# Optimization experiments

Hardware: AMD Instinct MI355X
Metric: run time of the kernel (lower is better)

The kernel has to match this reference:

```python
import jax, jax.numpy as jnp
import numpy as np

# static config (matches init_kwargs / input_specs)
B, S, D, H, DH = 4, 2048, 2048, 16, 128
MAX_LEN = 1024  # round_up_to_multiple_of_256(max ragged length); lengths below max at 1024
ROPE_BASE = 10000.0


def setup_inputs() -> dict:
    key = jax.random.key(0)
    ks = jax.random.split(key, 8)
    q_src = jax.random.normal(ks[0], (B, MAX_LEN, D), jnp.float32)
    k_src = jax.random.normal(ks[1], (B, S, D), jnp.float32)
    v_src = jax.random.normal(ks[2], (B, S, D), jnp.float32)
    std = 1.0 / np.sqrt(D)
    Wq = jax.random.normal(ks[3], (D, H * DH), jnp.float32) * std
    Wk = jax.random.normal(ks[4], (D, H * DH), jnp.float32) * std
    Wv = jax.random.normal(ks[5], (D, H * DH), jnp.float32) * std
    Wo = jax.random.normal(ks[6], (H * DH, D), jnp.float32) * (1.0 / np.sqrt(H * DH))
    # mask[0]: causal bool [B,S,S]; mask[1]: full position ids [B,S]
    mask0 = jnp.broadcast_to(jnp.tril(jnp.ones((S, S), bool)), (B, S, S))
    pos_full = jnp.broadcast_to(jnp.arange(S, dtype=jnp.int32), (B, S))
    # ragged skip_mask: row i keeps lengths[i] random positions (max 1024 -> MAX_LEN)
    lengths = jnp.array([1024, 896, 768, 640], jnp.int32)
    scores = jax.random.uniform(ks[7], (B, S))
    ranks = jnp.argsort(jnp.argsort(scores, axis=1), axis=1)
    skip_mask = ranks < lengths[:, None]
    return {"q_src": q_src, "k_src": k_src, "v_src": v_src,
            "Wq": Wq, "Wk": Wk, "Wv": Wv, "Wo": Wo,
            "mask0": mask0, "pos_full": pos_full, "skip_mask": skip_mask}


def _rope(x, positions):
    # x: [B,H,L,DH], positions: [B,L] int -> rotary embedding on full head dim
    dh = x.shape[-1]
    inv_freq = 1.0 / (ROPE_BASE ** (jnp.arange(0, dh, 2, dtype=jnp.float32) / dh))
    freqs = positions.astype(jnp.float32)[:, :, None] * inv_freq      # [B,L,dh/2]
    emb = jnp.concatenate([freqs, freqs], axis=-1)[:, None]           # [B,1,L,dh]
    x1, x2 = jnp.split(x, 2, axis=-1)
    rot = jnp.concatenate([-x2, x1], axis=-1)                         # rotate_half
    return x * jnp.cos(emb) + rot * jnp.sin(emb)


def reference(q_src, k_src, v_src, Wq, Wk, Wv, Wo, mask0, pos_full, skip_mask):
    def heads(x, W):
        y = x @ W
        return y.reshape(x.shape[0], x.shape[1], H, DH).transpose(0, 2, 1, 3)

    q = heads(q_src, Wq)   # [B,H,MAX_LEN,DH]
    k = heads(k_src, Wk)   # [B,H,S,DH]
    v = heads(v_src, Wv)   # [B,H,S,DH]

    # _trim_attention_mask: gather kept rows (True-first, stable order), pad to MAX_LEN
    order = jnp.argsort(jnp.where(skip_mask, 0, 1), axis=1)[:, :MAX_LEN]  # [B,MAX_LEN]
    n = skip_mask.sum(axis=1)                                             # ragged lengths
    valid = jnp.arange(MAX_LEN)[None, :] < n[:, None]                     # [B,MAX_LEN]
    amask = jnp.take_along_axis(mask0, order[:, :, None], axis=1) & valid[:, :, None]
    pos_trim = jnp.where(valid, jnp.take_along_axis(pos_full, order, axis=1), 0)

    # RoPE: trimmed positions for q, full positions for k
    q = _rope(q, pos_trim)
    k = _rope(k, pos_full)

    # masked SDPA; fully-masked (padded) query rows -> zero output
    logits = jnp.einsum('bhld,bhsd->bhls', q, k) / np.sqrt(DH).astype(np.float32)
    logits = jnp.where(amask[:, None], logits, jnp.finfo(logits.dtype).min)
    probs = jax.nn.softmax(logits, axis=-1) * valid[:, None, :, None]
    ctx = jnp.einsum('bhls,bhsd->bhld', probs, v)                         # [B,H,MAX_LEN,DH]

    out = ctx.transpose(0, 2, 1, 3).reshape(B, MAX_LEN, H * DH) @ Wo     # [B,MAX_LEN,D]
    return out
```

## Files before the change

kernel.cpp:

```cpp
#include <hip/hip_runtime.h>

#define BB 4
#define SS 2048
#define DD 2048
#define HH 16
#define DHD 128
#define MAXL 1024

typedef __bf16 bf16x8 __attribute__((ext_vector_type(8)));
typedef float f32x4 __attribute__((ext_vector_type(4)));
typedef unsigned int u32_as1 __attribute__((address_space(1)));
typedef unsigned int u32_as3 __attribute__((address_space(3)));

__device__ __forceinline__ unsigned short f2bf(float f) {
  unsigned int u = __builtin_bit_cast(unsigned int, f);
  u += 0x7fffu + ((u >> 16) & 1u);
  return (unsigned short)(u >> 16);
}
__device__ __forceinline__ float bf2f(unsigned short h) {
  unsigned int u = ((unsigned int)h) << 16;
  return __builtin_bit_cast(float, u);
}
union U4 { uint4 u; bf16x8 b; };
__device__ __forceinline__ bf16x8 ldfrag(const unsigned short* p) {
  U4 x; x.u = *(const uint4*)p; return x.b;
}
__device__ __forceinline__ void gl_lds16(const void* g, void* l) {
  __builtin_amdgcn_global_load_lds((const u32_as1*)g, (u32_as3*)l, 16, 0, 0);
}

template <int C>
__device__ __forceinline__ float dppf(float x) {
  return __builtin_bit_cast(float,
      __builtin_amdgcn_mov_dpp(__builtin_bit_cast(int, x), C, 0xF, 0xF, true));
}
__device__ __forceinline__ float rmax16(float x) {
  x = fmaxf(x, dppf<0xB1>(x));
  x = fmaxf(x, dppf<0x4E>(x));
  x = fmaxf(x, dppf<0x141>(x));
  x = fmaxf(x, dppf<0x140>(x));
  return x;
}
__device__ __forceinline__ float radd16(float x) {
  x += dppf<0xB1>(x);
  x += dppf<0x4E>(x);
  x += dppf<0x141>(x);
  x += dppf<0x140>(x);
  return x;
}

__global__ void build_pos(const int* __restrict__ skip, int* __restrict__ posk,
                          int* __restrict__ nval) {
  int b = blockIdx.x, t = threadIdx.x;
  __shared__ int cnts[64], offs[64];
  const int* row = skip + b * SS;
  int c = 0;
  for (int i = 0; i < 32; i++) c += (row[t * 32 + i] != 0);
  cnts[t] = c;
  __syncthreads();
  if (t == 0) {
    int run = 0;
    for (int i = 0; i < 64; i++) { offs[i] = run; run += cnts[i]; }
    nval[b] = run > MAXL ? MAXL : run;
  }
  __syncthreads();
  int o = offs[t];
  for (int i = 0; i < 32; i++)
    if (row[t * 32 + i]) { if (o < MAXL) posk[b * MAXL + o] = t * 32 + i; o++; }
  int nb = nval[b];
  for (int l = nb + t; l < MAXL; l += 64) posk[b * MAXL + l] = -1;
}

__global__ __launch_bounds__(256) void cvt3(const float* __restrict__ q,
                                            const float* __restrict__ k,
                                            const float* __restrict__ v,
                                            unsigned short* __restrict__ oq,
                                            unsigned short* __restrict__ ok,
                                            unsigned short* __restrict__ ov) {
  const int nq = BB * MAXL * DD / 4, nk = BB * SS * DD / 4;
  int idx = blockIdx.x * 256 + threadIdx.x;
  const float* src; unsigned short* dst; int off;
  if (idx < nq) { src = q; dst = oq; off = idx; }
  else if (idx < nq + nk) { src = k; dst = ok; off = idx - nq; }
  else { src = v; dst = ov; off = idx - nq - nk; }
  float4 vv = ((const float4*)src)[off];
  ushort4 h;
  h.x = f2bf(vv.x); h.y = f2bf(vv.y); h.z = f2bf(vv.z); h.w = f2bf(vv.w);
  ((ushort4*)dst)[off] = h;
}

__global__ __launch_bounds__(256) void transpose_w4(const float* __restrict__ w0,
    const float* __restrict__ w1, const float* __restrict__ w2, const float* __restrict__ w3,
    unsigned short* __restrict__ o0, unsigned short* __restrict__ o1,
    unsigned short* __restrict__ o2, unsigned short* __restrict__ o3) {
  __shared__ __align__(16) unsigned short tile[64 * 76];
  const float* W; unsigned short* Wt;
  switch (blockIdx.z) {
    case 0: W = w0; Wt = o0; break;
    case 1: W = w1; Wt = o1; break;
    case 2: W = w2; Wt = o2; break;
    default: W = w3; Wt = o3; break;
  }
  int tx = threadIdx.x;
  int K0 = blockIdx.y * 64, N0 = blockIdx.x * 64;
  #pragma unroll
  for (int i = 0; i < 4; i++) {
    int r = (tx >> 4) + i * 16, c4 = (tx & 15) * 4;
    float4 v = *(const float4*)&W[(size_t)(K0 + r) * DD + N0 + c4];
    ushort4 h;
    h.x = f2bf(v.x); h.y = f2bf(v.y); h.z = f2bf(v.z); h.w = f2bf(v.w);
    *(ushort4*)&tile[r * 76 + c4] = h;
  }
  __syncthreads();
  #pragma unroll
  for (int i = 0; i < 4; i++) {
    int n = (tx >> 4) + i * 16, k4 = (tx & 15) * 4;
    ushort4 h;
    h.x = tile[(k4 + 0) * 76 + n];
    h.y = tile[(k4 + 1) * 76 + n];
    h.z = tile[(k4 + 2) * 76 + n];
    h.w = tile[(k4 + 3) * 76 + n];
    *(ushort4*)&Wt[(size_t)(N0 + n) * DD + K0 + k4] = h;
  }
}

template <int BM>
__global__ __launch_bounds__(512, 2) void gemm8(const unsigned short* __restrict__ A,
                                                const unsigned short* __restrict__ Bt,
                                                void* __restrict__ Cp,
                                                int M, int N, int K, int mode, int Lbits) {
  constexpr int AFR = BM / 8;
  __shared__ __align__(16) unsigned short lds[(AFR + 32) * 1024];
  unsigned short* const Abuf = lds;
  unsigned short* const Bbuf = lds + 2 * AFR * 512;

  const int tid = threadIdx.x;
  const int lane = tid & 63, quad = lane >> 4, c = lane & 15;
  const int w = tid >> 6;
  const int wm = (w >> 2) * (BM / 2), wn = (w & 3) * 64;

  const int nwg = gridDim.x * gridDim.y;
  const int bid0 = blockIdx.y * gridDim.x + blockIdx.x;
  const int cpx = nwg >> 3;
  const int bid = (bid0 & 7) * cpx + (bid0 >> 3);
  const int bx = bid % gridDim.x;
  const int by = bid / gridDim.x;
  const size_t tm = (size_t)by * BM, tn = (size_t)bx * 256;

  constexpr int MR = BM / 32;
  f32x4 acc[MR][4] = {};

  constexpr int AN = AFR / 8;
  constexpr int NLD = AN + 4;
  const unsigned short* gA = A + (tm + c) * (size_t)K + quad * 8;
  const unsigned short* gB = Bt + (tn + c) * (size_t)K + quad * 8;

  auto STAGE = [&](int sel, int kk) {
    unsigned short* ad = Abuf + sel * (AFR * 512) + lane * 8;
    unsigned short* bd = Bbuf + sel * 16384 + lane * 8;
    #pragma unroll
    for (int n = 0; n < AN; n++) {
      int f = n * 8 + w;
      gl_lds16(gA + kk + ((size_t)(f >> 1) * 16) * K + (f & 1) * 32, ad + f * 512);
    }
    #pragma unroll
    for (int n = 0; n < 4; n++) {
      int f = n * 8 + w;
      gl_lds16(gB + kk + ((size_t)(f >> 1) * 16) * K + (f & 1) * 32, bd + f * 512);
    }
  };

  const int nkt = K >> 6;
  STAGE(0, 0);

  const int ai0 = (wm >> 4) * 2;
  const int bj0 = (wn >> 4) * 2;

  for (int t = 0; t < nkt; ++t) {
    const int sel = t & 1;
    const unsigned short* as = Abuf + sel * (AFR * 512) + lane * 8;
    const unsigned short* bs = Bbuf + sel * 16384 + lane * 8;
    if (t + 1 < nkt) {
      STAGE(sel ^ 1, (t + 1) << 6);
      asm volatile("s_waitcnt vmcnt(%0)" ::"i"(NLD) : "memory");
    } else {
      asm volatile("s_waitcnt vmcnt(0)" ::: "memory");
    }
    __builtin_amdgcn_s_barrier();

    bf16x8 a0[4][2], b01[2][2], b23[2][2];
    #pragma unroll
    for (int i = 0; i < 4; i++)
      #pragma unroll
      for (int ks = 0; ks < 2; ks++)
        a0[i][ks] = ldfrag(&as[(ai0 + i * 2 + ks) * 512]);
    #pragma unroll
    for (int j = 0; j < 2; j++)
      #pragma unroll
      for (int ks = 0; ks < 2; ks++)
        b01[j][ks] = ldfrag(&bs[(bj0 + j * 2 + ks) * 512]);
    __builtin_amdgcn_s_barrier();
    __builtin_amdgcn_s_setprio(1);
    #pragma unroll
    for (int i = 0; i < 4; i++)
      #pragma unroll
      for (int j = 0; j < 2; j++)
        #pragma unroll
        for (int ks = 0; ks < 2; ks++)
          acc[i][j] = __builtin_amdgcn_mfma_f32_16x16x32_bf16(a0[i][ks], b01[j][ks], acc[i][j], 0, 0, 0);
    __builtin_amdgcn_s_setprio(0);
    __builtin_amdgcn_s_barrier();
    #pragma unroll
    for (int j = 0; j < 2; j++)
      #pragma unroll
      for (int ks = 0; ks < 2; ks++)
        b23[j][ks] = ldfrag(&bs[(bj0 + (2 + j) * 2 + ks) * 512]);
    __builtin_amdgcn_s_barrier();
    __builtin_amdgcn_s_setprio(1);
    #pragma unroll
    for (int i = 0; i < 4; i++)
      #pragma unroll
      for (int j = 0; j < 2; j++)
        #pragma unroll
        for (int ks = 0; ks < 2; ks++)
          acc[i][2 + j] = __builtin_amdgcn_mfma_f32_16x16x32_bf16(a0[i][ks], b23[j][ks], acc[i][2 + j], 0, 0, 0);
    __builtin_amdgcn_s_setprio(0);
    __builtin_amdgcn_s_barrier();

    if constexpr (BM == 256) {
      bf16x8 a1[4][2];
      #pragma unroll
      for (int i = 0; i < 4; i++)
        #pragma unroll
        for (int ks = 0; ks < 2; ks++)
          a1[i][ks] = ldfrag(&as[(ai0 + (4 + i) * 2 + ks) * 512]);
      __builtin_amdgcn_s_barrier();
      __builtin_amdgcn_s_setprio(1);
      #pragma unroll
      for (int i = 0; i < 4; i++)
        #pragma unroll
        for (int j = 0; j < 2; j++)
          #pragma unroll
          for (int ks = 0; ks < 2; ks++)
            acc[4 + i][j] = __builtin_amdgcn_mfma_f32_16x16x32_bf16(a1[i][ks], b01[j][ks], acc[4 + i][j], 0, 0, 0);
      __builtin_amdgcn_s_setprio(0);
      __builtin_amdgcn_s_barrier();
      __builtin_amdgcn_s_setprio(1);
      #pragma unroll
      for (int i = 0; i < 4; i++)
        #pragma unroll
        for (int j = 0; j < 2; j++)
          #pragma unroll
          for (int ks = 0; ks < 2; ks++)
            acc[4 + i][2 + j] = __builtin_amdgcn_mfma_f32_16x16x32_bf16(a1[i][ks], b23[j][ks], acc[4 + i][2 + j], 0, 0, 0);
      __builtin_amdgcn_s_setprio(0);
      __builtin_amdgcn_s_barrier();
    }
  }

  if (mode == 1) {
    float* Cf = (float*)Cp;
    #pragma unroll
    for (int i = 0; i < MR; i++)
      #pragma unroll
      for (int j = 0; j < 4; j++)
        #pragma unroll
        for (int r = 0; r < 4; r++) {
          size_t m = tm + wm + i * 16 + quad * 4 + r;
          size_t n = tn + wn + j * 16 + c;
          Cf[m * N + n] = acc[i][j][r];
        }
    return;
  }
  unsigned short* Cb = (unsigned short*)Cp;
  unsigned short* ep = lds + w * 4352;
  constexpr int MH = BM / 128;
  if (mode == 0) {
    const size_t Lmask = ((size_t)1 << Lbits) - 1;
    #pragma unroll
    for (int mh = 0; mh < MH; mh++) {
      #pragma unroll
      for (int i = 0; i < 4; i++)
        #pragma unroll
        for (int j = 0; j < 4; j++)
          #pragma unroll
          for (int r = 0; r < 4; r++)
            ep[(i * 16 + quad * 4 + r) * 68 + j * 16 + c] = f2bf(acc[mh * 4 + i][j][r]);
      #pragma unroll
      for (int it = 0; it < 8; it++) {
        int chunk = it * 64 + lane;
        int ml = chunk >> 3, nc = (chunk & 7) * 8;
        uint4 val = *(const uint4*)&ep[ml * 68 + nc];
        size_t m = tm + wm + mh * 64 + ml, n = tn + wn + nc;
        size_t b = m >> Lbits, l = m & Lmask, h = n >> 7, d = n & 127;
        *(uint4*)&Cb[(((b * HH + h) << Lbits) + l) * 128 + d] = val;
      }
    }
  } else {
    #pragma unroll
    for (int mh = 0; mh < MH; mh++) {
      #pragma unroll
      for (int i = 0; i < 4; i++)
        #pragma unroll
        for (int j = 0; j < 4; j++)
          #pragma unroll
          for (int r = 0; r < 4; r++)
            ep[(j * 16 + c) * 68 + i * 16 + quad * 4 + r] = f2bf(acc[mh * 4 + i][j][r]);
      #pragma unroll
      for (int it = 0; it < 8; it++) {
        int chunk = it * 64 + lane;
        int nl = chunk >> 3, mc = (chunk & 7) * 8;
        uint4 val = *(const uint4*)&ep[nl * 68 + mc];
        size_t n = tn + wn + nl, m = tm + wm + mh * 64 + mc;
        size_t b = m >> 11, s = m & 2047, h = n >> 7, d = n & 127;
        *(uint4*)&Cb[((b * HH + h) * 128 + d) * SS + s] = val;
      }
    }
  }
}

__global__ __launch_bounds__(256) void rope2(unsigned short* __restrict__ xq,
                                             unsigned short* __restrict__ xk,
                                             const int* __restrict__ posk) {
  constexpr float QSCL = (float)(0.08838834764831843 * 1.4426950408889634);
  const int Nq = BB * HH * MAXL * 64;
  int gid = blockIdx.x * 256 + threadIdx.x;
  unsigned short* x; int Lbits, idx, use_posk;
  if (gid < Nq) { x = xq; Lbits = 10; use_posk = 1; idx = gid; }
  else { x = xk; Lbits = 11; use_posk = 0; idx = gid - Nq; }
  int d = idx & 63;
  int rest = idx >> 6;
  int l = rest & ((1 << Lbits) - 1);
  int bh = rest >> Lbits;
  int b = bh >> 4;
  int p = use_posk ? posk[(b << 10) + l] : l;
  float ang = (float)p * __expf(-(float)d * 0.14391156831212787f);
  float sn, cs;
  __sincosf(ang, &sn, &cs);
  float S = use_posk ? QSCL : 1.0f;
  size_t base = (size_t)rest * 128;
  float x1 = bf2f(x[base + d]), x2 = bf2f(x[base + d + 64]);
  x[base + d]      = f2bf((x1 * cs - x2 * sn) * S);
  x[base + d + 64] = f2bf((x2 * cs + x1 * sn) * S);
}

__global__ __launch_bounds__(256, 4) void attn_kernel(const unsigned short* __restrict__ qp,
                                                      const unsigned short* __restrict__ kp,
                                                      const unsigned short* __restrict__ vtp,
                                                      const int* __restrict__ posk,
                                                      const int* __restrict__ nval,
                                                      unsigned short* __restrict__ ctx) {
  __shared__ __align__(16) unsigned short k_s[8192];
  __shared__ __align__(16) unsigned short vt_s[8192];
  __shared__ __align__(16) unsigned short p_s[4096];

  const int tid = threadIdx.x;
  const int w = tid >> 6, lane = tid & 63, quad = lane >> 4, c = lane & 15;
  const int bh = blockIdx.x, b = bh >> 4, h = bh & 15;
  const int qbase = blockIdx.y * 64;
  const int nb = nval[b];
  const int* pb = posk + (b << 10) + qbase;

  int lv = nb - 1 - qbase; lv = lv > 63 ? 63 : lv;
  const int nkt = (lv >= 0) ? ((pb[lv] >> 6) + 1) : 0;
  const bool whas = (w * 16 <= lv);
  int wl = w * 16 + 15; if (wl > lv) wl = lv;
  const int wkmax = whas ? pb[wl] : -1;
  const int kminw = whas ? pb[w * 16] : -1;

  int km[4];
  #pragma unroll
  for (int r = 0; r < 4; r++) km[r] = pb[w * 16 + quad * 4 + r];

  const unsigned short* qg = qp + (((size_t)bh << 10) + qbase) * 128;
  bf16x8 aq[4];
  #pragma unroll
  for (int ks = 0; ks < 4; ks++)
    aq[ks] = ldfrag(&qg[(size_t)(w * 16 + c) * 128 + ks * 32 + quad * 8]);

  const unsigned short* kgp = kp + ((size_t)bh * SS + c) * 128 + (w * 4 + quad) * 8;
  auto STG_K = [&](int kb) {
    #pragma unroll
    for (int n = 0; n < 4; n++)
      gl_lds16(kgp + (size_t)(kb + n * 16) * 128, &k_s[(n * 4 + w) * 512 + lane * 8]);
  };
  auto STG_V = [&](int kb) {
    #pragma unroll
    for (int n = 0; n < 4; n++) {
      int f = n * 4 + w;
      gl_lds16(vtp + ((size_t)bh * 128 + (f >> 1) * 16 + c) * SS + kb + ((f & 1) * 4 + quad) * 8,
               &vt_s[f * 512 + lane * 8]);
    }
  };

  float m_i[4], l_i[4];
  #pragma unroll
  for (int r = 0; r < 4; r++) { m_i[r] = -1e30f; l_i[r] = 0.f; }
  f32x4 o[8];
  #pragma unroll
  for (int dj = 0; dj < 8; dj++) o[dj] = (f32x4){0.f, 0.f, 0.f, 0.f};

  const int pwb = w * 1024 + quad * 32 + (c & 7) + (c >> 3) * 128;

  if (nkt > 0) { STG_K(0); STG_V(0); }

  for (int kt = 0; kt < nkt; kt++) {
    const int kb = kt * 64;
    const bool more = (kt + 1 < nkt);
    asm volatile("s_waitcnt vmcnt(8)" ::: "memory");
    __builtin_amdgcn_s_barrier();

    const bool act = (kb <= wkmax);
    f32x4 sa[4];
    if (act) {
      #pragma unroll
      for (int j = 0; j < 4; j++) {
        sa[j] = (f32x4){0.f, 0.f, 0.f, 0.f};
        #pragma unroll
        for (int ks = 0; ks < 4; ks++) {
          bf16x8 bk = ldfrag(&k_s[(j * 4 + ks) * 512 + lane * 8]);
          sa[j] = __builtin_amdgcn_mfma_f32_16x16x32_bf16(aq[ks], bk, sa[j], 0, 0, 0);
        }
      }
    }
    __builtin_amdgcn_s_barrier();
    if (more) STG_K(kb + 64);

    if (act) {
      float mt[4] = {-1e30f, -1e30f, -1e30f, -1e30f};
      if (kb + 63 <= kminw) {
        #pragma unroll
        for (int j = 0; j < 4; j++)
          #pragma unroll
          for (int r = 0; r < 4; r++) mt[r] = fmaxf(mt[r], sa[j][r]);
      } else {
        #pragma unroll
        for (int j = 0; j < 4; j++) {
          int key = kb + j * 16 + c;
          #pragma unroll
          for (int r = 0; r < 4; r++) {
            float v = (key <= km[r]) ? sa[j][r] : -1e30f;
            sa[j][r] = v;
            mt[r] = fmaxf(mt[r], v);
          }
        }
      }
      float al[4], rs[4];
      #pragma unroll
      for (int r = 0; r < 4; r++) {
        mt[r] = rmax16(mt[r]);
        float mn = fmaxf(m_i[r], mt[r]);
        al[r] = __builtin_exp2f(m_i[r] - mn);
        m_i[r] = mn;
        rs[r] = 0.f;
      }
      #pragma unroll
      for (int j = 0; j < 4; j++)
        #pragma unroll
        for (int r = 0; r < 4; r++) {
          float pv = __builtin_exp2f(sa[j][r] - m_i[r]);
          sa[j][r] = pv;
          rs[r] += pv;
        }
      #pragma unroll
      for (int r = 0; r < 4; r++) {
        rs[r] = radd16(rs[r]);
        l_i[r] = l_i[r] * al[r] + rs[r];
      }
      #pragma unroll
      for (int dj = 0; dj < 8; dj++)
        #pragma unroll
        for (int r = 0; r < 4; r++) o[dj][r] *= al[r];
    }

    if (more) { asm volatile("s_waitcnt vmcnt(8)" ::: "memory"); }
    else      { asm volatile("s_waitcnt vmcnt(0)" ::: "memory"); }
    __builtin_amdgcn_s_barrier();

    if (act) {
      #pragma unroll
      for (int j = 0; j < 4; j++)
        #pragma unroll
        for (int r = 0; r < 4; r++)
          p_s[pwb + (j >> 1) * 512 + (j & 1) * 256 + r * 8] = f2bf(sa[j][r]);
      #pragma unroll
      for (int ks2 = 0; ks2 < 2; ks2++) {
        bf16x8 ap = ldfrag(&p_s[(w * 2 + ks2) * 512 + lane * 8]);
        #pragma unroll
        for (int dj = 0; dj < 8; dj++) {
          bf16x8 bv = ldfrag(&vt_s[(dj * 2 + ks2) * 512 + lane * 8]);
          o[dj] = __builtin_amdgcn_mfma_f32_16x16x32_bf16(ap, bv, o[dj], 0, 0, 0);
        }
      }
    }
    __builtin_amdgcn_s_barrier();
    if (more) STG_V(kb + 64);
  }

  #pragma unroll
  for (int r = 0; r < 4; r++) {
    int l = qbase + w * 16 + quad * 4 + r;
    bool ok = (l < nb);
    float inv = ok ? (1.0f / l_i[r]) : 0.0f;
    #pragma unroll
    for (int dj = 0; dj < 8; dj++)
      ctx[(((size_t)b << 10) + l) * (size_t)DD + h * 128 + dj * 16 + c] =
          f2bf(ok ? o[dj][r] * inv : 0.0f);
  }
}

extern "C" void kernel_launch(void* const* d_in, const int* in_sizes, int n_in,
                              void* d_out, int out_size, void* d_ws, size_t ws_size,
                              hipStream_t stream) {
  const float* q_src = (const float*)d_in[0];
  const float* k_src = (const float*)d_in[1];
  const float* v_src = (const float*)d_in[2];
  const float* Wq = (const float*)d_in[3];
  const float* Wk = (const float*)d_in[4];
  const float* Wv = (const float*)d_in[5];
  const float* Wo = (const float*)d_in[6];
  const int* skip = (const int*)d_in[9];

  char* p = (char*)d_ws;
  auto alloc = [&](size_t bytes) -> char* {
    char* r = p;
    p += (bytes + 255) & ~(size_t)255;
    return r;
  };
  unsigned short* a_q  = (unsigned short*)alloc((size_t)BB * MAXL * DD * 2);
  unsigned short* a_k  = (unsigned short*)alloc((size_t)BB * SS * DD * 2);
  unsigned short* a_v  = (unsigned short*)alloc((size_t)BB * SS * DD * 2);
  unsigned short* wt_q = (unsigned short*)alloc((size_t)DD * DD * 2);
  unsigned short* wt_k = (unsigned short*)alloc((size_t)DD * DD * 2);
  unsigned short* wt_v = (unsigned short*)alloc((size_t)DD * DD * 2);
  unsigned short* wt_o = (unsigned short*)alloc((size_t)DD * DD * 2);
  unsigned short* q_pro = (unsigned short*)alloc((size_t)BB * HH * MAXL * DHD * 2);
  unsigned short* k_pro = (unsigned short*)alloc((size_t)BB * HH * SS * DHD * 2);
  unsigned short* v_t   = (unsigned short*)alloc((size_t)BB * HH * SS * DHD * 2);
  int* posk = (int*)alloc((size_t)BB * MAXL * 4);
  int* nval = (int*)alloc(64);
  unsigned short* ctx = a_q;

  build_pos<<<BB, 64, 0, stream>>>(skip, posk, nval);
  cvt3<<<(BB * MAXL * DD + 2 * BB * SS * DD) / (4 * 256), 256, 0, stream>>>(
      q_src, k_src, v_src, a_q, a_k, a_v);
  transpose_w4<<<dim3(32, 32, 4), 256, 0, stream>>>(Wq, Wk, Wv, Wo, wt_q, wt_k, wt_v, wt_o);

  gemm8<128><<<dim3(8, 32), 512, 0, stream>>>(a_q, wt_q, q_pro, BB * MAXL, DD, DD, 0, 10);
  gemm8<256><<<dim3(8, 32), 512, 0, stream>>>(a_k, wt_k, k_pro, BB * SS, DD, DD, 0, 11);
  gemm8<256><<<dim3(8, 32), 512, 0, stream>>>(a_v, wt_v, v_t, BB * SS, DD, DD, 2, 11);

  rope2<<<(BB * HH * (MAXL + SS) * 64) / 256, 256, 0, stream>>>(q_pro, k_pro, posk);

  attn_kernel<<<dim3(BB * HH, MAXL / 64), 256, 0, stream>>>(q_pro, k_pro, v_t, posk, nval, ctx);

  gemm8<128><<<dim3(8, 32), 512, 0, stream>>>(ctx, wt_o, d_out, BB * MAXL, DD, DD, 1, 0);
}
```

Before: 809.3 us.

## Add 256x256 quadrant GEMM for K/V projections and double-buffer attention K/V

Adds a new gemm256q kernel that computes 256x256 output tiles in four quadrants, interleaving next-tile global-to-LDS loads between quadrant MFMA phases. The K and V projections now use it, and gemm8 is trimmed to the BM=128 path. The attention kernel gets double-buffered K and V LDS tiles with a single combined prefetch per iteration, drops intermediate barriers, and caches per-row key limits in shared memory. The aim is to overlap memory loads with MFMA work and cut synchronisation, at the cost of more LDS per block, which may reduce occupancy.

```diff
diff --git a/kernel.cpp b/kernel.cpp
--- a/kernel.cpp
+++ b/kernel.cpp
@@ -124,6 +124,162 @@
   }
 }
 
+template <int MODE>
+__global__ __launch_bounds__(512, 2) void gemm256q(const unsigned short* __restrict__ A,
+                                                   const unsigned short* __restrict__ Bt,
+                                                   unsigned short* __restrict__ Cb,
+                                                   int K, int Lbits) {
+  __shared__ __align__(16) unsigned short lds[65536];
+  unsigned short* const Abuf = lds;
+  unsigned short* const Bbuf = lds + 32768;
+
+  const int tid = threadIdx.x;
+  const int lane = tid & 63, quad = lane >> 4, c = lane & 15;
+  const int w = tid >> 6;
+  const int wr = w >> 2, wc = w & 3;
+
+  const int nwg = gridDim.x * gridDim.y;
+  const int bid0 = blockIdx.y * gridDim.x + blockIdx.x;
+  const int cpx = nwg >> 3;
+  const int bid = (bid0 & 7) * cpx + (bid0 >> 3);
+  const int bx = bid % gridDim.x;
+  const int by = bid / gridDim.x;
+  const size_t tm = (size_t)by * 256, tn = (size_t)bx * 256;
+
+  f32x4 acc[4][4][2] = {};
+
+  auto STG_A = [&](int sel, int tk, int half) {
+    int rg = half * 8 + w;
+    const unsigned short* src = A + (tm + rg * 16 + c) * (size_t)K + tk * 64 + quad * 8;
+    unsigned short* dst = Abuf + sel * 16384 + (rg * 2) * 512 + lane * 8;
+    gl_lds16(src, dst);
+    gl_lds16(src + 32, dst + 512);
+  };
+  auto STG_B = [&](int sel, int tk, int half) {
+    int rg = half * 8 + w;
+    const unsigned short* src = Bt + (tn + rg * 16 + c) * (size_t)K + tk * 64 + quad * 8;
+    unsigned short* dst = Bbuf + sel * 16384 + (rg * 2) * 512 + lane * 8;
+    gl_lds16(src, dst);
+    gl_lds16(src + 32, dst + 512);
+  };
+
+  const int nkt = K >> 6;
+  STG_A(0, 0, 0);
+  STG_B(0, 0, 0);
+  STG_B(0, 0, 1);
+  STG_A(0, 0, 1);
+
+  bf16x8 av[4][2], b01[2][2], b23[2][2];
+
+#define MFMA_Q(QI, AV, BV)                                                         \
+  __builtin_amdgcn_s_setprio(1);                                                   \
+  _Pragma("unroll")                                                                \
+  for (int i = 0; i < 4; i++)                                                      \
+    _Pragma("unroll")                                                              \
+    for (int j = 0; j < 2; j++)                                                    \
+      _Pragma("unroll")                                                            \
+      for (int ks = 0; ks < 2; ks++)                                               \
+        acc[QI][i][j] = __builtin_amdgcn_mfma_f32_16x16x32_bf16(                   \
+            AV[i][ks], BV[j][ks], acc[QI][i][j], 0, 0, 0);                         \
+  __builtin_amdgcn_s_setprio(0);
+
+  for (int t = 0; t < nkt; ++t) {
+    const int sel = t & 1, ns = sel ^ 1;
+    const unsigned short* as = Abuf + sel * 16384 + lane * 8;
+    const unsigned short* bs = Bbuf + sel * 16384 + lane * 8;
+    const bool more = (t + 1 < nkt);
+
+    if (more) { STG_A(ns, t + 1, 0); asm volatile("s_waitcnt vmcnt(6)" ::: "memory"); }
+    else      {                       asm volatile("s_waitcnt vmcnt(4)" ::: "memory"); }
+    __builtin_amdgcn_s_barrier();
+    #pragma unroll
+    for (int i = 0; i < 4; i++)
+      #pragma unroll
+      for (int ks = 0; ks < 2; ks++)
+        av[i][ks] = ldfrag(&as[((wr * 4 + i) * 2 + ks) * 512]);
+    #pragma unroll
+    for (int j = 0; j < 2; j++)
+      #pragma unroll
+      for (int ks = 0; ks < 2; ks++)
+        b01[j][ks] = ldfrag(&bs[((wc * 2 + j) * 2 + ks) * 512]);
+    MFMA_Q(0, av, b01)
+    __builtin_amdgcn_s_barrier();
+
+    if (more) { STG_B(ns, t + 1, 0); asm volatile("s_waitcnt vmcnt(6)" ::: "memory"); }
+    else      {                       asm volatile("s_waitcnt vmcnt(2)" ::: "memory"); }
+    __builtin_amdgcn_s_barrier();
+    #pragma unroll
+    for (int j = 0; j < 2; j++)
+      #pragma unroll
+      for (int ks = 0; ks < 2; ks++)
+        b23[j][ks] = ldfrag(&bs[((8 + wc * 2 + j) * 2 + ks) * 512]);
+    MFMA_Q(1, av, b23)
+    __builtin_amdgcn_s_barrier();
+
+    if (more) { STG_B(ns, t + 1, 1); asm volatile("s_waitcnt vmcnt(6)" ::: "memory"); }
+    else      {                       asm volatile("s_waitcnt vmcnt(0)" ::: "memory"); }
+    __builtin_amdgcn_s_barrier();
+    #pragma unroll
+    for (int i = 0; i < 4; i++)
+      #pragma unroll
+      for (int ks = 0; ks < 2; ks++)
+        av[i][ks] = ldfrag(&as[((8 + wr * 4 + i) * 2 + ks) * 512]);
+    MFMA_Q(2, av, b01)
+    __builtin_amdgcn_s_barrier();
+
+    if (more) STG_A(ns, t + 1, 1);
+    MFMA_Q(3, av, b23)
+    __builtin_amdgcn_s_barrier();
+  }
+#undef MFMA_Q
+
+  unsigned short* ep = lds + w * 2048;
+  const size_t Lmask = ((size_t)1 << Lbits) - 1;
+  #pragma unroll
+  for (int qm = 0; qm < 2; qm++)
+    #pragma unroll
+    for (int qn = 0; qn < 2; qn++) {
+      const int qi = qm * 2 + qn;
+      if (MODE == 0) {
+        #pragma unroll
+        for (int i = 0; i < 4; i++)
+          #pragma unroll
+          for (int j = 0; j < 2; j++)
+            #pragma unroll
+            for (int r = 0; r < 4; r++)
+              ep[(i * 16 + quad * 4 + r) * 32 + j * 16 + c] = f2bf(acc[qi][i][j][r]);
+        #pragma unroll
+        for (int it = 0; it < 4; it++) {
+          int idx = it * 64 + lane;
+          int row = idx >> 2, cc = (idx & 3) * 8;
+          uint4 val = *(const uint4*)&ep[row * 32 + cc];
+          size_t m = tm + qm * 128 + wr * 64 + row;
+          size_t n = tn + qn * 128 + wc * 32 + cc;
+          size_t b = m >> Lbits, l = m & Lmask, h = n >> 7, d = n & 127;
+          *(uint4*)&Cb[(((b * HH + h) << Lbits) + l) * 128 + d] = val;
+        }
+      } else {
+        #pragma unroll
+        for (int i = 0; i < 4; i++)
+          #pragma unroll
+          for (int j = 0; j < 2; j++)
+            #pragma unroll
+            for (int r = 0; r < 4; r++)
+              ep[(j * 16 + c) * 64 + i * 16 + quad * 4 + r] = f2bf(acc[qi][i][j][r]);
+        #pragma unroll
+        for (int it = 0; it < 4; it++) {
+          int idx = it * 64 + lane;
+          int nl = idx >> 3, mc = (idx & 7) * 8;
+          uint4 val = *(const uint4*)&ep[nl * 64 + mc];
+          size_t n = tn + qn * 128 + wc * 32 + nl;
+          size_t m = tm + qm * 128 + wr * 64 + mc;
+          size_t b = m >> 11, s = m & 2047, h = n >> 7, d = n & 127;
+          *(uint4*)&Cb[((b * HH + h) * 128 + d) * SS + s] = val;
+        }
+      }
+    }
+}
+
 template <int BM>
 __global__ __launch_bounds__(512, 2) void gemm8(const unsigned short* __restrict__ A,
                                                 const unsigned short* __restrict__ Bt,
@@ -226,36 +382,6 @@
           acc[i][2 + j] = __builtin_amdgcn_mfma_f32_16x16x32_bf16(a0[i][ks], b23[j][ks], acc[i][2 + j], 0, 0, 0);
     __builtin_amdgcn_s_setprio(0);
     __builtin_amdgcn_s_barrier();
-
-    if constexpr (BM == 256) {
-      bf16x8 a1[4][2];
-      #pragma unroll
-      for (int i = 0; i < 4; i++)
-        #pragma unroll
-        for (int ks = 0; ks < 2; ks++)
-          a1[i][ks] = ldfrag(&as[(ai0 + (4 + i) * 2 + ks) * 512]);
-      __builtin_amdgcn_s_barrier();
-      __builtin_amdgcn_s_setprio(1);
-      #pragma unroll
-      for (int i = 0; i < 4; i++)
-        #pragma unroll
-        for (int j = 0; j < 2; j++)
-          #pragma unroll
-          for (int ks = 0; ks < 2; ks++)
-            acc[4 + i][j] = __builtin_amdgcn_mfma_f32_16x16x32_bf16(a1[i][ks], b01[j][ks], acc[4 + i][j], 0, 0, 0);
-      __builtin_amdgcn_s_setprio(0);
-      __builtin_amdgcn_s_barrier();
-      __builtin_amdgcn_s_setprio(1);
-      #pragma unroll
-      for (int i = 0; i < 4; i++)
-        #pragma unroll
-        for (int j = 0; j < 2; j++)
-          #pragma unroll
-          for (int ks = 0; ks < 2; ks++)
-            acc[4 + i][2 + j] = __builtin_amdgcn_mfma_f32_16x16x32_bf16(a1[i][ks], b23[j][ks], acc[4 + i][2 + j], 0, 0, 0);
-      __builtin_amdgcn_s_setprio(0);
-      __builtin_amdgcn_s_barrier();
-    }
   }
 
   if (mode == 1) {
@@ -274,48 +400,22 @@
   }
   unsigned short* Cb = (unsigned short*)Cp;
   unsigned short* ep = lds + w * 4352;
-  constexpr int MH = BM / 128;
-  if (mode == 0) {
-    const size_t Lmask = ((size_t)1 << Lbits) - 1;
-    #pragma unroll
-    for (int mh = 0; mh < MH; mh++) {
-      #pragma unroll
-      for (int i = 0; i < 4; i++)
-        #pragma unroll
-        for (int j = 0; j < 4; j++)
-          #pragma unroll
-          for (int r = 0; r < 4; r++)
-            ep[(i * 16 + quad * 4 + r) * 68 + j * 16 + c] = f2bf(acc[mh * 4 + i][j][r]);
-      #pragma unroll
-      for (int it = 0; it < 8; it++) {
-        int chunk = it * 64 + lane;
-        int ml = chunk >> 3, nc = (chunk & 7) * 8;
-        uint4 val = *(const uint4*)&ep[ml * 68 + nc];
-        size_t m = tm + wm + mh * 64 + ml, n = tn + wn + nc;
-        size_t b = m >> Lbits, l = m & Lmask, h = n >> 7, d = n & 127;
-        *(uint4*)&Cb[(((b * HH + h) << Lbits) + l) * 128 + d] = val;
-      }
-    }
-  } else {
-    #pragma unroll
-    for (int mh = 0; mh < MH; mh++) {
-      #pragma unroll
-      for (int i = 0; i < 4; i++)
-        #pragma unroll
-        for (int j = 0; j < 4; j++)
-          #pragma unroll
-          for (int r = 0; r < 4; r++)
-            ep[(j * 16 + c) * 68 + i * 16 + quad * 4 + r] = f2bf(acc[mh * 4 + i][j][r]);
-      #pragma unroll
-      for (int it = 0; it < 8; it++) {
-        int chunk = it * 64 + lane;
-        int nl = chunk >> 3, mc = (chunk & 7) * 8;
-        uint4 val = *(const uint4*)&ep[nl * 68 + mc];
-        size_t n = tn + wn + nl, m = tm + wm + mh * 64 + mc;
-        size_t b = m >> 11, s = m & 2047, h = n >> 7, d = n & 127;
-        *(uint4*)&Cb[((b * HH + h) * 128 + d) * SS + s] = val;
-      }
-    }
+  const size_t Lmask = ((size_t)1 << Lbits) - 1;
+  #pragma unroll
+  for (int i = 0; i < 4; i++)
+    #pragma unroll
+    for (int j = 0; j < 4; j++)
+      #pragma unroll
+      for (int r = 0; r < 4; r++)
+        ep[(i * 16 + quad * 4 + r) * 68 + j * 16 + c] = f2bf(acc[i][j][r]);
+  #pragma unroll
+  for (int it = 0; it < 8; it++) {
+    int chunk = it * 64 + lane;
+    int ml = chunk >> 3, nc = (chunk & 7) * 8;
+    uint4 val = *(const uint4*)&ep[ml * 68 + nc];
+    size_t m = tm + wm + ml, n = tn + wn + nc;
+    size_t b = m >> Lbits, l = m & Lmask, h = n >> 7, d = n & 127;
+    *(uint4*)&Cb[(((b * HH + h) << Lbits) + l) * 128 + d] = val;
   }
 }
 
@@ -344,52 +444,57 @@
   x[base + d + 64] = f2bf((x2 * cs + x1 * sn) * S);
 }
 
-__global__ __launch_bounds__(256, 4) void attn_kernel(const unsigned short* __restrict__ qp,
-                                                      const unsigned short* __restrict__ kp,
-                                                      const unsigned short* __restrict__ vtp,
-                                                      const int* __restrict__ posk,
-                                                      const int* __restrict__ nval,
-                                                      unsigned short* __restrict__ ctx) {
-  __shared__ __align__(16) unsigned short k_s[8192];
-  __shared__ __align__(16) unsigned short vt_s[8192];
+__global__ __launch_bounds__(256) void attn_kernel(const unsigned short* __restrict__ qp,
+                                                   const unsigned short* __restrict__ kp,
+                                                   const unsigned short* __restrict__ vtp,
+                                                   const int* __restrict__ posk,
+                                                   const int* __restrict__ nval,
+                                                   unsigned short* __restrict__ ctx) {
+  __shared__ __align__(16) unsigned short k_s[2][8192];
+  __shared__ __align__(16) unsigned short vt_s[2][8192];
   __shared__ __align__(16) unsigned short p_s[4096];
+  __shared__ int km_s[64];
 
   const int tid = threadIdx.x;
   const int w = tid >> 6, lane = tid & 63, quad = lane >> 4, c = lane & 15;
   const int bh = blockIdx.x, b = bh >> 4, h = bh & 15;
   const int qbase = blockIdx.y * 64;
   const int nb = nval[b];
-  const int* pb = posk + (b << 10) + qbase;
+
+  if (tid < 64) {
+    int l = qbase + tid;
+    km_s[tid] = (l < nb) ? posk[(b << 10) + l] : -1;
+  }
+  __syncthreads();
 
   int lv = nb - 1 - qbase; lv = lv > 63 ? 63 : lv;
-  const int nkt = (lv >= 0) ? ((pb[lv] >> 6) + 1) : 0;
+  const int tile_kmax = (lv >= 0) ? km_s[lv] : -1;
+  const int nkt = (tile_kmax >= 0) ? ((tile_kmax >> 6) + 1) : 0;
   const bool whas = (w * 16 <= lv);
   int wl = w * 16 + 15; if (wl > lv) wl = lv;
-  const int wkmax = whas ? pb[wl] : -1;
-  const int kminw = whas ? pb[w * 16] : -1;
-
+  const int wkmax = whas ? km_s[wl] : -1;
+  const int kminw = whas ? km_s[w * 16] : -1;
   int km[4];
   #pragma unroll
-  for (int r = 0; r < 4; r++) km[r] = pb[w * 16 + quad * 4 + r];
+  for (int r = 0; r < 4; r++) km[r] = km_s[w * 16 + quad * 4 + r];
 
   const unsigned short* qg = qp + (((size_t)bh << 10) + qbase) * 128;
   bf16x8 aq[4];
   #pragma unroll
   for (int ks = 0; ks < 4; ks++)
     aq[ks] = ldfrag(&qg[(size_t)(w * 16 + c) * 128 + ks * 32 + quad * 8]);
+  asm volatile("" : "+v"(aq[0]), "+v"(aq[1]), "+v"(aq[2]), "+v"(aq[3]) :: "memory");
 
   const unsigned short* kgp = kp + ((size_t)bh * SS + c) * 128 + (w * 4 + quad) * 8;
-  auto STG_K = [&](int kb) {
+  auto STG = [&](int buf, int kb) {
     #pragma unroll
     for (int n = 0; n < 4; n++)
-      gl_lds16(kgp + (size_t)(kb + n * 16) * 128, &k_s[(n * 4 + w) * 512 + lane * 8]);
-  };
-  auto STG_V = [&](int kb) {
+      gl_lds16(kgp + (size_t)(kb + n * 16) * 128, &k_s[buf][(n * 4 + w) * 512 + lane * 8]);
     #pragma unroll
     for (int n = 0; n < 4; n++) {
       int f = n * 4 + w;
       gl_lds16(vtp + ((size_t)bh * 128 + (f >> 1) * 16 + c) * SS + kb + ((f & 1) * 4 + quad) * 8,
-               &vt_s[f * 512 + lane * 8]);
+               &vt_s[buf][f * 512 + lane * 8]);
     }
   };
 
@@ -402,31 +507,31 @@
 
   const int pwb = w * 1024 + quad * 32 + (c & 7) + (c >> 3) * 128;
 
-  if (nkt > 0) { STG_K(0); STG_V(0); }
+  if (nkt > 0) STG(0, 0);
 
   for (int kt = 0; kt < nkt; kt++) {
+    const int cur = kt & 1;
     const int kb = kt * 64;
-    const bool more = (kt + 1 < nkt);
-    asm volatile("s_waitcnt vmcnt(8)" ::: "memory");
-    __builtin_amdgcn_s_barrier();
-
-    const bool act = (kb <= wkmax);
-    f32x4 sa[4];
-    if (act) {
+    if (kt + 1 < nkt) {
+      STG(cur ^ 1, kb + 64);
+      asm volatile("s_waitcnt vmcnt(8)" ::: "memory");
+    } else {
+      asm volatile("s_waitcnt vmcnt(0)" ::: "memory");
+    }
+    __builtin_amdgcn_s_barrier();
+
+    if (kb <= wkmax) {
+      f32x4 sa[4];
       #pragma unroll
       for (int j = 0; j < 4; j++) {
         sa[j] = (f32x4){0.f, 0.f, 0.f, 0.f};
         #pragma unroll
         for (int ks = 0; ks < 4; ks++) {
-          bf16x8 bk = ldfrag(&k_s[(j * 4 + ks) * 512 + lane * 8]);
+          bf16x8 bk = ldfrag(&k_s[cur][(j * 4 + ks) * 512 + lane * 8]);
           sa[j] = __builtin_amdgcn_mfma_f32_16x16x32_bf16(aq[ks], bk, sa[j], 0, 0, 0);
         }
       }
-    }
-    __builtin_amdgcn_s_barrier();
-    if (more) STG_K(kb + 64);
-
-    if (act) {
+
       float mt[4] = {-1e30f, -1e30f, -1e30f, -1e30f};
       if (kb + 63 <= kminw) {
         #pragma unroll
@@ -471,13 +576,7 @@
       for (int dj = 0; dj < 8; dj++)
         #pragma unroll
         for (int r = 0; r < 4; r++) o[dj][r] *= al[r];
-    }
-
-    if (more) { asm volatile("s_waitcnt vmcnt(8)" ::: "memory"); }
-    else      { asm volatile("s_waitcnt vmcnt(0)" ::: "memory"); }
-    __builtin_amdgcn_s_barrier();
-
-    if (act) {
+
       #pragma unroll
       for (int j = 0; j < 4; j++)
         #pragma unroll
@@ -488,13 +587,12 @@
         bf16x8 ap = ldfrag(&p_s[(w * 2 + ks2) * 512 + lane * 8]);
         #pragma unroll
         for (int dj = 0; dj < 8; dj++) {
-          bf16x8 bv = ldfrag(&vt_s[(dj * 2 + ks2) * 512 + lane * 8]);
+          bf16x8 bv = ldfrag(&vt_s[cur][(dj * 2 + ks2) * 512 + lane * 8]);
           o[dj] = __builtin_amdgcn_mfma_f32_16x16x32_bf16(ap, bv, o[dj], 0, 0, 0);
         }
       }
     }
     __builtin_amdgcn_s_barrier();
-    if (more) STG_V(kb + 64);
   }
 
   #pragma unroll
@@ -547,8 +645,8 @@
   transpose_w4<<<dim3(32, 32, 4), 256, 0, stream>>>(Wq, Wk, Wv, Wo, wt_q, wt_k, wt_v, wt_o);
 
   gemm8<128><<<dim3(8, 32), 512, 0, stream>>>(a_q, wt_q, q_pro, BB * MAXL, DD, DD, 0, 10);
-  gemm8<256><<<dim3(8, 32), 512, 0, stream>>>(a_k, wt_k, k_pro, BB * SS, DD, DD, 0, 11);
-  gemm8<256><<<dim3(8, 32), 512, 0, stream>>>(a_v, wt_v, v_t, BB * SS, DD, DD, 2, 11);
+  gemm256q<0><<<dim3(8, 32), 512, 0, stream>>>(a_k, wt_k, k_pro, DD, 11);
+  gemm256q<2><<<dim3(8, 32), 512, 0, stream>>>(a_v, wt_v, v_t, DD, 11);
 
   rope2<<<(BB * HH * (MAXL + SS) * 64) / 256, 256, 0, stream>>>(q_pro, k_pro, posk);
 
```

After: 834.1 us. 1.03x slower.
